# Performance work log

Measured on AMD Instinct MI355X. Metric: run time of the kernel, lower is better.

Reference implementation:

```python
import jax, jax.numpy as jnp
import numpy as np

D_MODEL = 512
D_INNER = 1024   # expand * d_model
D_STATE = 16
D_CONV = 4
DT_RANK = 32     # ceil(d_model / 16)
N_LAYERS = 4
N_PRED_LAYERS = 2
FEAT = 128
LN_EPS = 1e-5


def _ln(x, w, b):
    m = x.mean(-1, keepdims=True)
    v = ((x - m) ** 2).mean(-1, keepdims=True)
    return (x - m) * jax.lax.rsqrt(v + LN_EPS) * w + b


def _silu(x):
    return x * jax.nn.sigmoid(x)


def _causal_conv(x, w, b):
    # depthwise causal conv1d: x (B,L,C), w (C,K), b (C,)
    K = w.shape[1]
    L = x.shape[1]
    xp = jnp.pad(x, ((0, 0), (K - 1, 0), (0, 0)))
    y = b
    for k in range(K):
        y = y + xp[:, k:k + L, :] * w[:, k]
    return y


def _mamba(x, in_w, conv_w, conv_b, xp_w, dt_w, dt_b, Alog, Dp, out_w):
    # x: (B,L,d_model)
    xz = jnp.einsum('bld,ed->ble', x, in_w)          # (B,L,2*d_inner)
    xi, z = jnp.split(xz, 2, axis=-1)
    xc = _silu(_causal_conv(xi, conv_w, conv_b))     # (B,L,d_inner)
    dbc = jnp.einsum('blc,ec->ble', xc, xp_w)        # (B,L,dt_rank+2N)
    dt = dbc[..., :DT_RANK]
    Bm = dbc[..., DT_RANK:DT_RANK + D_STATE]         # (B,L,N)
    Cm = dbc[..., DT_RANK + D_STATE:]                # (B,L,N)
    delta = jax.nn.softplus(jnp.einsum('blr,cr->blc', dt, dt_w) + dt_b)  # (B,L,d_inner)
    A = -jnp.exp(Alog)                               # (d_inner,N), negative
    dA = jnp.exp(delta[..., None] * A)               # (B,L,d_inner,N)
    dBu = delta[..., None] * Bm[:, :, None, :] * xc[..., None]

    def step(h, inp):
        dA_t, dBu_t, C_t = inp
        h = dA_t * h + dBu_t                         # (B,d_inner,N)
        y = jnp.einsum('bcn,bn->bc', h, C_t)
        return h, y

    h0 = jnp.zeros((x.shape[0], D_INNER, D_STATE), x.dtype)
    _, ys = jax.lax.scan(step, h0, (dA.transpose(1, 0, 2, 3),
                                    dBu.transpose(1, 0, 2, 3),
                                    Cm.transpose(1, 0, 2)))
    y = ys.transpose(1, 0, 2) + Dp * xc              # skip connection D*u
    y = y * _silu(z)
    return jnp.einsum('blc,dc->bld', y, out_w)


def _forward(x, inp_w, inp_b, enc_ln_w, enc_ln_b, enc_in_w, enc_conv_w, enc_conv_b,
             enc_xp_w, enc_dt_w, enc_dt_b, enc_Alog, enc_D, enc_out_w,
             fin_ln_w, fin_ln_b, prd_ln_w, prd_ln_b, prd_in_w, prd_conv_w, prd_conv_b,
             prd_xp_w, prd_dt_w, prd_dt_b, prd_Alog, prd_D, prd_out_w,
             prd_nrm_w, prd_nrm_b, prd_proj_w, prd_proj_b):
    # MambaEncoder: input_proj + n_layers pre-norm residual Mamba blocks + final LN
    h = jnp.einsum('blf,df->bld', x, inp_w) + inp_b
    for i in range(N_LAYERS):
        h = h + _mamba(_ln(h, enc_ln_w[i], enc_ln_b[i]),
                       enc_in_w[i], enc_conv_w[i], enc_conv_b[i], enc_xp_w[i],
                       enc_dt_w[i], enc_dt_b[i], enc_Alog[i], enc_D[i], enc_out_w[i])
    ctx = _ln(h, fin_ln_w, fin_ln_b)
    # MambaPredictor: small causal mamba stack + norm + proj
    p = ctx
    for i in range(N_PRED_LAYERS):
        p = p + _mamba(_ln(p, prd_ln_w[i], prd_ln_b[i]),
                       prd_in_w[i], prd_conv_w[i], prd_conv_b[i], prd_xp_w[i],
                       prd_dt_w[i], prd_dt_b[i], prd_Alog[i], prd_D[i], prd_out_w[i])
    p = _ln(p, prd_nrm_w, prd_nrm_b)
    preds = jnp.einsum('bld,ed->ble', p, prd_proj_w) + prd_proj_b
    return preds


def _mamba_params(key, n, scale=0.02):
    ks = jax.random.split(key, 6)
    arange_A = jnp.tile(jnp.log(jnp.arange(1, D_STATE + 1, dtype=jnp.float32)), (n, D_INNER, 1))
    return dict(
        in_w=jax.random.normal(ks[0], (n, 2 * D_INNER, D_MODEL)) * scale,
        conv_w=jax.random.normal(ks[1], (n, D_INNER, D_CONV)) * scale,
        conv_b=jnp.zeros((n, D_INNER)),
        xp_w=jax.random.normal(ks[2], (n, DT_RANK + 2 * D_STATE, D_INNER)) * scale,
        dt_w=jax.random.normal(ks[3], (n, D_INNER, DT_RANK)) * scale,
        dt_b=jnp.full((n, D_INNER), jnp.log(jnp.expm1(0.01))),  # inv-softplus(0.01)
        Alog=arange_A,
        D=jnp.ones((n, D_INNER)),
        out_w=jax.random.normal(ks[4], (n, D_MODEL, D_INNER)) * scale,
    )


def setup_inputs() -> dict:
    key = jax.random.key(0)
    ks = jax.random.split(key, 8)
    enc = _mamba_params(ks[0], N_LAYERS)
    prd = _mamba_params(ks[1], N_PRED_LAYERS)
    return {
        'x': jax.random.normal(ks[2], (2, 1024, FEAT), dtype=jnp.float32),
        'inp_w': jax.random.normal(ks[3], (D_MODEL, FEAT)) * 0.02,
        'inp_b': jnp.zeros((D_MODEL,)),
        'enc_ln_w': jnp.ones((N_LAYERS, D_MODEL)), 'enc_ln_b': jnp.zeros((N_LAYERS, D_MODEL)),
        'enc_in_w': enc['in_w'], 'enc_conv_w': enc['conv_w'], 'enc_conv_b': enc['conv_b'],
        'enc_xp_w': enc['xp_w'], 'enc_dt_w': enc['dt_w'], 'enc_dt_b': enc['dt_b'],
        'enc_Alog': enc['Alog'], 'enc_D': enc['D'], 'enc_out_w': enc['out_w'],
        'fin_ln_w': jnp.ones((D_MODEL,)), 'fin_ln_b': jnp.zeros((D_MODEL,)),
        'prd_ln_w': jnp.ones((N_PRED_LAYERS, D_MODEL)), 'prd_ln_b': jnp.zeros((N_PRED_LAYERS, D_MODEL)),
        'prd_in_w': prd['in_w'], 'prd_conv_w': prd['conv_w'], 'prd_conv_b': prd['conv_b'],
        'prd_xp_w': prd['xp_w'], 'prd_dt_w': prd['dt_w'], 'prd_dt_b': prd['dt_b'],
        'prd_Alog': prd['Alog'], 'prd_D': prd['D'], 'prd_out_w': prd['out_w'],
        'prd_nrm_w': jnp.ones((D_MODEL,)), 'prd_nrm_b': jnp.zeros((D_MODEL,)),
        'prd_proj_w': jax.random.normal(ks[4], (D_MODEL, D_MODEL)) * 0.02,
        'prd_proj_b': jnp.zeros((D_MODEL,)),
    }


def reference(x, inp_w, inp_b, enc_ln_w, enc_ln_b, enc_in_w, enc_conv_w, enc_conv_b,
              enc_xp_w, enc_dt_w, enc_dt_b, enc_Alog, enc_D, enc_out_w,
              fin_ln_w, fin_ln_b, prd_ln_w, prd_ln_b, prd_in_w, prd_conv_w, prd_conv_b,
              prd_xp_w, prd_dt_w, prd_dt_b, prd_Alog, prd_D, prd_out_w,
              prd_nrm_w, prd_nrm_b, prd_proj_w, prd_proj_b):
    return _forward(x, inp_w, inp_b, enc_ln_w, enc_ln_b, enc_in_w, enc_conv_w, enc_conv_b,
                    enc_xp_w, enc_dt_w, enc_dt_b, enc_Alog, enc_D, enc_out_w,
                    fin_ln_w, fin_ln_b, prd_ln_w, prd_ln_b, prd_in_w, prd_conv_w, prd_conv_b,
                    prd_xp_w, prd_dt_w, prd_dt_b, prd_Alog, prd_D, prd_out_w,
                    prd_nrm_w, prd_nrm_b, prd_proj_w, prd_proj_b)
```

## Files before the change

### kernel.cpp

```cpp
#include <hip/hip_runtime.h>
#include <hip/hip_bf16.h>

using bf16 = __hip_bfloat16;
typedef __attribute__((ext_vector_type(8))) short short8;
typedef __attribute__((ext_vector_type(4))) float f32x4;

static constexpr int LB = 2;
static constexpr int LL = 1024;
static constexpr int DM = 512;
static constexpr int DI = 1024;
static constexpr int DSN = 16;
static constexpr int RK = 32;
static constexpr int MR_ROWS = LB * LL;

static constexpr int NCHUNK = 64;
static constexpr int CH = LL / NCHUNK;

__device__ __forceinline__ void gload16(const void* g, void* l) {
    __builtin_amdgcn_global_load_lds(
        (__attribute__((address_space(1))) void*)(g),
        (__attribute__((address_space(3))) void*)(l), 16, 0, 0);
}

struct ConvArgs {
    const float* src[9];
    bf16*        dst[9];
    int          n4[9];
};

__global__ __launch_bounds__(256) void convert_bf16_multi(ConvArgs a) {
    const int s = blockIdx.y;
    const float4* __restrict__ src = (const float4*)a.src[s];
    bf16* __restrict__ dst = a.dst[s];
    const int n4 = a.n4[s];
    for (int i = blockIdx.x * 256 + threadIdx.x; i < n4; i += gridDim.x * 256) {
        float4 v = src[i];
        bf16 t[4] = {__float2bfloat16(v.x), __float2bfloat16(v.y),
                     __float2bfloat16(v.z), __float2bfloat16(v.w)};
        *(uint2*)(dst + (size_t)i * 4) = *(uint2*)t;
    }
}

__global__ __launch_bounds__(256) void transpose_dtw(const float* __restrict__ enc_dtw,
                                                     const float* __restrict__ prd_dtw,
                                                     float* __restrict__ out) {
    const int layer = blockIdx.y;
    const float* src = (layer < 4) ? enc_dtw + (size_t)layer * DI * RK
                                   : prd_dtw + (size_t)(layer - 4) * DI * RK;
    float* dst = out + (size_t)layer * RK * DI;
    const int idx = blockIdx.x * 256 + threadIdx.x;
    const int k = idx >> 10, c = idx & (DI - 1);
    dst[idx] = src[(size_t)c * RK + k];
}

__device__ __forceinline__ void ln_store8(float* outrow, int lane,
                                          const float* v) {
    float4 a = {v[0], v[1], v[2], v[3]}, b = {v[4], v[5], v[6], v[7]};
    ((float4*)outrow)[lane] = a;
    ((float4*)outrow)[lane + 64] = b;
}
__device__ __forceinline__ void ln_store8(bf16* outrow, int lane,
                                          const float* v) {
    bf16 t0[4] = {__float2bfloat16(v[0]), __float2bfloat16(v[1]),
                  __float2bfloat16(v[2]), __float2bfloat16(v[3])};
    bf16 t1[4] = {__float2bfloat16(v[4]), __float2bfloat16(v[5]),
                  __float2bfloat16(v[6]), __float2bfloat16(v[7])};
    ((uint2*)outrow)[lane] = *(uint2*)t0;
    ((uint2*)outrow)[lane + 64] = *(uint2*)t1;
}

template <typename T>
__global__ __launch_bounds__(256) void ln_kernel(const float* __restrict__ x,
                                                 const float* __restrict__ w,
                                                 const float* __restrict__ b,
                                                 T* __restrict__ out,
                                                 float* __restrict__ dbc_zero) {
    if (dbc_zero != nullptr && blockIdx.x < 128) {
        ((float4*)dbc_zero)[blockIdx.x * 256 + threadIdx.x] =
            make_float4(0.f, 0.f, 0.f, 0.f);
    }
    const int wid = threadIdx.x >> 6, lane = threadIdx.x & 63;
    const int row = blockIdx.x * 4 + wid;
    const float4* xr = (const float4*)(x + (size_t)row * DM);
    const float4 v0 = xr[lane], v1 = xr[lane + 64];

    float s = (v0.x + v0.y + v0.z + v0.w) + (v1.x + v1.y + v1.z + v1.w);
#pragma unroll
    for (int m = 1; m < 64; m <<= 1) s += __shfl_xor(s, m);
    const float mean = s * (1.f / DM);

    float d[8] = {v0.x - mean, v0.y - mean, v0.z - mean, v0.w - mean,
                  v1.x - mean, v1.y - mean, v1.z - mean, v1.w - mean};
    float s2 = 0.f;
#pragma unroll
    for (int q = 0; q < 8; ++q) s2 += d[q] * d[q];
#pragma unroll
    for (int m = 1; m < 64; m <<= 1) s2 += __shfl_xor(s2, m);
    const float rs = rsqrtf(s2 * (1.f / DM) + 1e-5f);

    const float4 w0 = ((const float4*)w)[lane], w1 = ((const float4*)w)[lane + 64];
    const float4 b0 = ((const float4*)b)[lane], b1 = ((const float4*)b)[lane + 64];
    float o[8] = {d[0] * rs * w0.x + b0.x, d[1] * rs * w0.y + b0.y,
                  d[2] * rs * w0.z + b0.z, d[3] * rs * w0.w + b0.w,
                  d[4] * rs * w1.x + b1.x, d[5] * rs * w1.y + b1.y,
                  d[6] * rs * w1.z + b1.z, d[7] * rs * w1.w + b1.w};
    ln_store8(out + (size_t)row * DM, lane, o);
}

template <int BM, int BN, int BK, int EPI>
__global__ __launch_bounds__(256) void gemm_bt(const bf16* __restrict__ A, int lda,
                                               const bf16* __restrict__ B, int ldb,
                                               float* __restrict__ C, int ldc,
                                               int K, const float* __restrict__ bias) {
    static_assert(BK == 64, "layout assumes 128B LDS row");
    static_assert(BM % 32 == 0 && BN % 32 == 0, "wave staging granularity");
    constexpr int MR = (BM / 2) / 16;
    constexpr int NR = (BN / 2) / 16;
    __shared__ __align__(16) char sA[BM * 128];
    __shared__ __align__(16) char sB[BN * 128];

    const int tid = threadIdx.x;
    const int lane = tid & 63, wid = tid >> 6;
    const int wr = wid >> 1, wc = wid & 1;
    const int m0 = blockIdx.y * BM, n0 = blockIdx.x * BN;
    const int kbase = (EPI == 2) ? blockIdx.z * K : 0;

    f32x4 acc[MR][NR] = {};

    const int lrow = lane >> 3;
    const int lcol = (lane & 7) ^ lrow;
    const size_t lda2 = (size_t)lda * 2, ldb2 = (size_t)ldb * 2;
    const char* Ab = (const char*)A + (size_t)(m0 + wid * (BM / 4) + lrow) * lda2
                     + lcol * 16 + (size_t)kbase * 2;
    const char* Bb = (const char*)B + (size_t)(n0 + wid * (BN / 4) + lrow) * ldb2
                     + lcol * 16 + (size_t)kbase * 2;
    char* sAw = sA + wid * (BM / 4) * 128;
    char* sBw = sB + wid * (BN / 4) * 128;

    for (int k0 = 0; k0 < K; k0 += BK) {
#pragma unroll
        for (int i = 0; i < BM / 32; ++i)
            gload16(Ab + (size_t)i * 8 * lda2 + (size_t)k0 * 2, sAw + i * 1024);
#pragma unroll
        for (int i = 0; i < BN / 32; ++i)
            gload16(Bb + (size_t)i * 8 * ldb2 + (size_t)k0 * 2, sBw + i * 1024);
        __syncthreads();
#pragma unroll
        for (int kk = 0; kk < BK; kk += 32) {
            const int kb2 = (kk + (lane >> 4) * 8) * 2;
            short8 af[MR], bfr[NR];
#pragma unroll
            for (int m = 0; m < MR; ++m) {
                const int r = wr * (BM / 2) + m * 16 + (lane & 15);
                af[m] = *(const short8*)(sA + r * 128 + (kb2 ^ ((r & 7) << 4)));
            }
#pragma unroll
            for (int n = 0; n < NR; ++n) {
                const int r = wc * (BN / 2) + n * 16 + (lane & 15);
                bfr[n] = *(const short8*)(sB + r * 128 + (kb2 ^ ((r & 7) << 4)));
            }
#pragma unroll
            for (int m = 0; m < MR; ++m) {
#pragma unroll
                for (int n = 0; n < NR; ++n) {
                    acc[m][n] = __builtin_amdgcn_mfma_f32_16x16x32_bf16(af[m], bfr[n], acc[m][n], 0, 0, 0);
                }
            }
        }
        __syncthreads();
    }

#pragma unroll
    for (int m = 0; m < MR; ++m) {
#pragma unroll
        for (int n = 0; n < NR; ++n) {
            const int col = n0 + wc * (BN / 2) + n * 16 + (lane & 15);
            const float bv = (EPI == 1) ? bias[col] : 0.f;
#pragma unroll
            for (int j = 0; j < 4; ++j) {
                const int row = m0 + wr * (BM / 2) + m * 16 + (lane >> 4) * 4 + j;
                float v = acc[m][n][j] + bv;
                if (EPI == 4) {
                    ((bf16*)C)[(size_t)row * ldc + col] = __float2bfloat16(v);
                } else {
                    float* p = C + (size_t)row * ldc + col;
                    if (EPI == 2) {
                        atomicAdd(p, v);
                    } else {
                        if (EPI == 3) v += *p;
                        *p = v;
                    }
                }
            }
        }
    }
}

__global__ __launch_bounds__(256) void conv_silu_b(const bf16* __restrict__ xzb,
                                                   const float* __restrict__ cw,
                                                   const float* __restrict__ cb,
                                                   bf16* __restrict__ xc_bf) {
    const int idx = blockIdx.x * 256 + threadIdx.x;
    const int c = idx & (DI - 1);
    const int r = idx >> 10;
    const int l = r & (LL - 1);
    const bf16* xi = xzb + (size_t)r * (2 * DI) + c;
    const float4 w = *(const float4*)(cw + (size_t)c * 4);
    float acc = cb[c] + w.w * __bfloat162float(xi[0]);
    if (l >= 1) acc += w.z * __bfloat162float(xi[-(2 * DI)]);
    if (l >= 2) acc += w.y * __bfloat162float(xi[-(4 * DI)]);
    if (l >= 3) acc += w.x * __bfloat162float(xi[-(6 * DI)]);
    const float s = acc / (1.f + expf(-acc));
    xc_bf[idx] = __float2bfloat16(s);
}

__global__ __launch_bounds__(256) void scan_part1(const bf16* __restrict__ xcb,
                                                  const float* __restrict__ dbc,
                                                  const float* __restrict__ Alog,
                                                  const float* __restrict__ dtw_t,
                                                  const float* __restrict__ dtb,
                                                  float* __restrict__ psum,
                                                  float* __restrict__ ssum) {
    const int lane = threadIdx.x & 63;
    const int wsub = threadIdx.x >> 6;
    const int c = blockIdx.x * 64 + lane;
    const int chunk = blockIdx.y * 4 + wsub;
    const int b = blockIdx.z;
    const int r0 = b * LL + chunk * CH;

    float wv[RK];
#pragma unroll
    for (int k = 0; k < RK; ++k) wv[k] = dtw_t[(size_t)k * DI + c];
    const float bdt = dtb[c];

    float a2[DSN];
#pragma unroll
    for (int q = 0; q < 4; ++q) {
        const float4 al = *(const float4*)(Alog + (size_t)c * DSN + q * 4);
        a2[q * 4 + 0] = -expf(al.x) * 1.44269504f;
        a2[q * 4 + 1] = -expf(al.y) * 1.44269504f;
        a2[q * 4 + 2] = -expf(al.z) * 1.44269504f;
        a2[q * 4 + 3] = -expf(al.w) * 1.44269504f;
    }

    float h[DSN], P[DSN];
#pragma unroll
    for (int n = 0; n < DSN; ++n) { h[n] = 0.f; P[n] = 1.f; }

    for (int t = 0; t < CH; ++t) {
        const size_t r = r0 + t;
        float acc = bdt;
#pragma unroll
        for (int q = 0; q < RK / 4; ++q) {
            const float4 d4 = *(const float4*)(dbc + r * 64 + q * 4);
            acc = fmaf(d4.x, wv[q * 4 + 0], acc);
            acc = fmaf(d4.y, wv[q * 4 + 1], acc);
            acc = fmaf(d4.z, wv[q * 4 + 2], acc);
            acc = fmaf(d4.w, wv[q * 4 + 3], acc);
        }
        const float d = (acc > 20.f) ? acc : log1pf(expf(acc));

        const float xv = __bfloat162float(xcb[r * DI + c]);
        const float dxv = d * xv;
        float Bv[DSN];
#pragma unroll
        for (int q = 0; q < 4; ++q)
            *(float4*)&Bv[q * 4] = *(const float4*)(dbc + r * 64 + 32 + q * 4);
#pragma unroll
        for (int n = 0; n < DSN; ++n) {
            const float dA = exp2f(d * a2[n]);
            h[n] = fmaf(dA, h[n], dxv * Bv[n]);
            P[n] *= dA;
        }
    }

    const size_t obase = ((size_t)(b * NCHUNK + chunk) * DSN) * DI + c;
#pragma unroll
    for (int n = 0; n < DSN; ++n) {
        psum[obase + (size_t)n * DI] = P[n];
        ssum[obase + (size_t)n * DI] = h[n];
    }
}

__global__ __launch_bounds__(256) void scan_combine(float* __restrict__ psum,
                                                    const float* __restrict__ ssum) {
    const int lane = threadIdx.x & 63;
    const int idx = blockIdx.y * 4 + (threadIdx.x >> 6);
    const int b = idx >> 4, n = idx & 15;
    const int c = blockIdx.x * 64 + lane;
    const size_t base = ((size_t)(b * NCHUNK) * DSN + n) * DI + c;
    const size_t stride = (size_t)DSN * DI;

    float h = 0.f;
    for (int j0 = 0; j0 < NCHUNK; j0 += 8) {
        float Pv[8], Sv[8];
#pragma unroll
        for (int u = 0; u < 8; ++u) {
            Pv[u] = psum[base + (j0 + u) * stride];
            Sv[u] = ssum[base + (j0 + u) * stride];
        }
#pragma unroll
        for (int u = 0; u < 8; ++u) {
            psum[base + (j0 + u) * stride] = h;
            h = fmaf(Pv[u], h, Sv[u]);
        }
    }
}

__global__ __launch_bounds__(256) void scan_part3(const bf16* __restrict__ xcb,
                                                  const bf16* __restrict__ xzb,
                                                  const float* __restrict__ dbc,
                                                  const float* __restrict__ Alog,
                                                  const float* __restrict__ dtw_t,
                                                  const float* __restrict__ dtb,
                                                  const float* __restrict__ Dp,
                                                  const float* __restrict__ hin,
                                                  bf16* __restrict__ yg) {
    const int lane = threadIdx.x & 63;
    const int wsub = threadIdx.x >> 6;
    const int c = blockIdx.x * 64 + lane;
    const int chunk = blockIdx.y * 4 + wsub;
    const int b = blockIdx.z;
    const int r0 = b * LL + chunk * CH;

    float wv[RK];
#pragma unroll
    for (int k = 0; k < RK; ++k) wv[k] = dtw_t[(size_t)k * DI + c];
    const float bdt = dtb[c];

    float a2[DSN];
#pragma unroll
    for (int q = 0; q < 4; ++q) {
        const float4 al = *(const float4*)(Alog + (size_t)c * DSN + q * 4);
        a2[q * 4 + 0] = -expf(al.x) * 1.44269504f;
        a2[q * 4 + 1] = -expf(al.y) * 1.44269504f;
        a2[q * 4 + 2] = -expf(al.z) * 1.44269504f;
        a2[q * 4 + 3] = -expf(al.w) * 1.44269504f;
    }
    const float dp = Dp[c];

    float h[DSN];
    const size_t hbase = ((size_t)(b * NCHUNK + chunk) * DSN) * DI + c;
#pragma unroll
    for (int n = 0; n < DSN; ++n) h[n] = hin[hbase + (size_t)n * DI];

    for (int t = 0; t < CH; ++t) {
        const size_t r = r0 + t;
        float acc = bdt;
#pragma unroll
        for (int q = 0; q < RK / 4; ++q) {
            const float4 d4 = *(const float4*)(dbc + r * 64 + q * 4);
            acc = fmaf(d4.x, wv[q * 4 + 0], acc);
            acc = fmaf(d4.y, wv[q * 4 + 1], acc);
            acc = fmaf(d4.z, wv[q * 4 + 2], acc);
            acc = fmaf(d4.w, wv[q * 4 + 3], acc);
        }
        const float d = (acc > 20.f) ? acc : log1pf(expf(acc));

        const float xv = __bfloat162float(xcb[r * DI + c]);
        const float zv = __bfloat162float(xzb[r * (2 * DI) + DI + c]);
        const float dxv = d * xv;
        float Bv[DSN], Cv[DSN];
#pragma unroll
        for (int q = 0; q < 4; ++q) {
            *(float4*)&Bv[q * 4] = *(const float4*)(dbc + r * 64 + 32 + q * 4);
            *(float4*)&Cv[q * 4] = *(const float4*)(dbc + r * 64 + 48 + q * 4);
        }
        float y0 = 0.f, y1 = 0.f, y2 = 0.f, y3 = 0.f;
#pragma unroll
        for (int q = 0; q < 4; ++q) {
            {
                const float dA = exp2f(d * a2[q * 4 + 0]);
                h[q * 4 + 0] = fmaf(dA, h[q * 4 + 0], dxv * Bv[q * 4 + 0]);
                y0 = fmaf(h[q * 4 + 0], Cv[q * 4 + 0], y0);
            }
            {
                const float dA = exp2f(d * a2[q * 4 + 1]);
                h[q * 4 + 1] = fmaf(dA, h[q * 4 + 1], dxv * Bv[q * 4 + 1]);
                y1 = fmaf(h[q * 4 + 1], Cv[q * 4 + 1], y1);
            }
            {
                const float dA = exp2f(d * a2[q * 4 + 2]);
                h[q * 4 + 2] = fmaf(dA, h[q * 4 + 2], dxv * Bv[q * 4 + 2]);
                y2 = fmaf(h[q * 4 + 2], Cv[q * 4 + 2], y2);
            }
            {
                const float dA = exp2f(d * a2[q * 4 + 3]);
                h[q * 4 + 3] = fmaf(dA, h[q * 4 + 3], dxv * Bv[q * 4 + 3]);
                y3 = fmaf(h[q * 4 + 3], Cv[q * 4 + 3], y3);
            }
        }
        const float y = (y0 + y1) + (y2 + y3);
        const float zs = zv / (1.f + expf(-zv));
        yg[r * DI + c] = __float2bfloat16((y + dp * xv) * zs);
    }
}

static void run_mamba_layer(hipStream_t stream, float* resid,
                            const float* ln_w, const float* ln_b,
                            const bf16* inw_bf,
                            const float* conv_w, const float* conv_b,
                            const bf16* xpw_bf,
                            const float* dtw_t, const float* dt_b,
                            const float* Alog, const float* Dp,
                            const bf16* outw_bf,
                            bf16* ln_bf, bf16* xzb, bf16* xc_bf, float* dbc,
                            float* psum, float* ssum, bf16* yg_bf) {
    ln_kernel<bf16><<<MR_ROWS / 4, 256, 0, stream>>>(resid, ln_w, ln_b, ln_bf, dbc);
    gemm_bt<64, 64, 64, 4><<<dim3(2 * DI / 64, MR_ROWS / 64), 256, 0, stream>>>(
        ln_bf, DM, inw_bf, DM, (float*)xzb, 2 * DI, DM, nullptr);
    conv_silu_b<<<MR_ROWS * DI / 256, 256, 0, stream>>>(xzb, conv_w, conv_b, xc_bf);
    gemm_bt<32, 64, 64, 2><<<dim3(1, MR_ROWS / 32, 4), 256, 0, stream>>>(
        xc_bf, DI, xpw_bf, DI, dbc, 64, DI / 4, nullptr);
    scan_part1<<<dim3(DI / 64, NCHUNK / 4, LB), 256, 0, stream>>>(
        xc_bf, dbc, Alog, dtw_t, dt_b, psum, ssum);
    scan_combine<<<dim3(DI / 64, (LB * DSN) / 4), 256, 0, stream>>>(psum, ssum);
    scan_part3<<<dim3(DI / 64, NCHUNK / 4, LB), 256, 0, stream>>>(
        xc_bf, xzb, dbc, Alog, dtw_t, dt_b, Dp, psum, yg_bf);
    gemm_bt<32, 64, 64, 3><<<dim3(DM / 64, MR_ROWS / 32), 256, 0, stream>>>(
        yg_bf, DI, outw_bf, DI, resid, DM, DI, nullptr);
}

extern "C" void kernel_launch(void* const* d_in, const int* in_sizes, int n_in,
                              void* d_out, int out_size, void* d_ws, size_t ws_size,
                              hipStream_t stream) {
    const float* x         = (const float*)d_in[0];
    const float* inp_w     = (const float*)d_in[1];
    const float* inp_b     = (const float*)d_in[2];
    const float* enc_ln_w  = (const float*)d_in[3];
    const float* enc_ln_b  = (const float*)d_in[4];
    const float* enc_in_w  = (const float*)d_in[5];
    const float* enc_conv_w= (const float*)d_in[6];
    const float* enc_conv_b= (const float*)d_in[7];
    const float* enc_xp_w  = (const float*)d_in[8];
    const float* enc_dt_w  = (const float*)d_in[9];
    const float* enc_dt_b  = (const float*)d_in[10];
    const float* enc_Alog  = (const float*)d_in[11];
    const float* enc_D     = (const float*)d_in[12];
    const float* enc_out_w = (const float*)d_in[13];
    const float* fin_ln_w  = (const float*)d_in[14];
    const float* fin_ln_b  = (const float*)d_in[15];
    const float* prd_ln_w  = (const float*)d_in[16];
    const float* prd_ln_b  = (const float*)d_in[17];
    const float* prd_in_w  = (const float*)d_in[18];
    const float* prd_conv_w= (const float*)d_in[19];
    const float* prd_conv_b= (const float*)d_in[20];
    const float* prd_xp_w  = (const float*)d_in[21];
    const float* prd_dt_w  = (const float*)d_in[22];
    const float* prd_dt_b  = (const float*)d_in[23];
    const float* prd_Alog  = (const float*)d_in[24];
    const float* prd_D     = (const float*)d_in[25];
    const float* prd_out_w = (const float*)d_in[26];
    const float* prd_nrm_w = (const float*)d_in[27];
    const float* prd_nrm_b = (const float*)d_in[28];
    const float* prd_proj_w= (const float*)d_in[29];
    const float* prd_proj_b= (const float*)d_in[30];

    char* wp = (char*)d_ws;
    auto carve = [&](size_t elems, size_t esz) {
        void* p = (void*)wp;
        wp += (elems * esz + 255) & ~(size_t)255;
        return p;
    };
    bf16* x_bf     = (bf16*)carve((size_t)MR_ROWS * 128, 2);
    bf16* inpw_bf  = (bf16*)carve((size_t)DM * 128, 2);
    bf16* einw_bf  = (bf16*)carve(4ull * 2 * DI * DM, 2);
    bf16* expw_bf  = (bf16*)carve(4ull * 64 * DI, 2);
    bf16* eoutw_bf = (bf16*)carve(4ull * DM * DI, 2);
    bf16* pinw_bf  = (bf16*)carve(2ull * 2 * DI * DM, 2);
    bf16* pxpw_bf  = (bf16*)carve(2ull * 64 * DI, 2);
    bf16* poutw_bf = (bf16*)carve(2ull * DM * DI, 2);
    bf16* projw_bf = (bf16*)carve((size_t)DM * DM, 2);
    float* dtwt    = (float*)carve(6ull * RK * DI, 4);
    float* hbuf    = (float*)carve((size_t)MR_ROWS * DM, 4);
    float* pbuf    = (float*)carve((size_t)MR_ROWS * DM, 4);
    bf16* ln_bf    = (bf16*)carve((size_t)MR_ROWS * DM, 2);
    bf16* xzb      = (bf16*)carve((size_t)MR_ROWS * 2 * DI, 2);
    bf16* xc_bf    = (bf16*)carve((size_t)MR_ROWS * DI, 2);
    float* dbc     = (float*)carve((size_t)MR_ROWS * 64, 4);
    float* psum    = (float*)carve((size_t)LB * NCHUNK * DSN * DI, 4);
    float* ssum    = (float*)carve((size_t)LB * NCHUNK * DSN * DI, 4);
    bf16* yg_bf    = (bf16*)carve((size_t)MR_ROWS * DI, 2);

    ConvArgs ca;
    const float* csrc[9] = {x, inp_w, enc_in_w, enc_xp_w, enc_out_w,
                            prd_in_w, prd_xp_w, prd_out_w, prd_proj_w};
    bf16* cdst[9] = {x_bf, inpw_bf, einw_bf, expw_bf, eoutw_bf,
                     pinw_bf, pxpw_bf, poutw_bf, projw_bf};
    const int cn[9] = {MR_ROWS * 128, DM * 128, 4 * 2 * DI * DM, 4 * 64 * DI, 4 * DM * DI,
                       2 * 2 * DI * DM, 2 * 64 * DI, 2 * DM * DI, DM * DM};
    for (int i = 0; i < 9; ++i) { ca.src[i] = csrc[i]; ca.dst[i] = cdst[i]; ca.n4[i] = cn[i] / 4; }
    convert_bf16_multi<<<dim3(128, 9), 256, 0, stream>>>(ca);
    transpose_dtw<<<dim3(RK * DI / 256, 6), 256, 0, stream>>>(enc_dt_w, prd_dt_w, dtwt);

    gemm_bt<32, 64, 64, 1><<<dim3(DM / 64, MR_ROWS / 32), 256, 0, stream>>>(
        x_bf, 128, inpw_bf, 128, hbuf, DM, 128, inp_b);

    for (int i = 0; i < 4; ++i) {
        run_mamba_layer(stream, hbuf,
                        enc_ln_w + (size_t)i * DM, enc_ln_b + (size_t)i * DM,
                        einw_bf + (size_t)i * 2 * DI * DM,
                        enc_conv_w + (size_t)i * DI * 4, enc_conv_b + (size_t)i * DI,
                        expw_bf + (size_t)i * 64 * DI,
                        dtwt + (size_t)i * RK * DI, enc_dt_b + (size_t)i * DI,
                        enc_Alog + (size_t)i * DI * DSN, enc_D + (size_t)i * DI,
                        eoutw_bf + (size_t)i * DM * DI,
                        ln_bf, xzb, xc_bf, dbc, psum, ssum, yg_bf);
    }

    ln_kernel<float><<<MR_ROWS / 4, 256, 0, stream>>>(hbuf, fin_ln_w, fin_ln_b, pbuf, nullptr);

    for (int i = 0; i < 2; ++i) {
        run_mamba_layer(stream, pbuf,
                        prd_ln_w + (size_t)i * DM, prd_ln_b + (size_t)i * DM,
                        pinw_bf + (size_t)i * 2 * DI * DM,
                        prd_conv_w + (size_t)i * DI * 4, prd_conv_b + (size_t)i * DI,
                        pxpw_bf + (size_t)i * 64 * DI,
                        dtwt + (size_t)(4 + i) * RK * DI, prd_dt_b + (size_t)i * DI,
                        prd_Alog + (size_t)i * DI * DSN, prd_D + (size_t)i * DI,
                        poutw_bf + (size_t)i * DM * DI,
                        ln_bf, xzb, xc_bf, dbc, psum, ssum, yg_bf);
    }

    ln_kernel<bf16><<<MR_ROWS / 4, 256, 0, stream>>>(pbuf, prd_nrm_w, prd_nrm_b, ln_bf, nullptr);
    gemm_bt<32, 64, 64, 1><<<dim3(DM / 64, MR_ROWS / 32), 256, 0, stream>>>(
        ln_bf, DM, projw_bf, DM, (float*)d_out, DM, DM, prd_proj_b);

    (void)in_sizes; (void)n_in; (void)out_size; (void)ws_size;
}
```

Before: 660.6 us.

## Fuse conv, x_proj GEMM and chunked scan into one cooperative persistent kernel

Replaces five launches per layer (conv+silu, split-K x_proj GEMM, scan part1, combine, part3) with a single cooperative kernel of 512 blocks that runs each stage in turn, with grid.sync between stages. The dbc zeroing moves from the layernorm kernel into the fused kernel. The aim is to remove launch overhead and inter-kernel gaps across six layers. In exchange, grid-wide barriers add cost, the x_proj stage now uses small 16-row tiles with one loading wave, and the grid is fixed at 512 blocks, so it must stay co-resident (launch bounds set to two blocks per CU).

```diff
diff --git a/kernel.cpp b/kernel.cpp
--- a/kernel.cpp
+++ b/kernel.cpp
@@ -1,5 +1,8 @@
 #include <hip/hip_runtime.h>
 #include <hip/hip_bf16.h>
+#include <hip/hip_cooperative_groups.h>
+
+namespace cg = cooperative_groups;
 
 using bf16 = __hip_bfloat16;
 typedef __attribute__((ext_vector_type(8))) short short8;
@@ -73,12 +76,7 @@
 __global__ __launch_bounds__(256) void ln_kernel(const float* __restrict__ x,
                                                  const float* __restrict__ w,
                                                  const float* __restrict__ b,
-                                                 T* __restrict__ out,
-                                                 float* __restrict__ dbc_zero) {
-    if (dbc_zero != nullptr && blockIdx.x < 128) {
-        ((float4*)dbc_zero)[blockIdx.x * 256 + threadIdx.x] =
-            make_float4(0.f, 0.f, 0.f, 0.f);
-    }
+                                                 T* __restrict__ out) {
     const int wid = threadIdx.x >> 6, lane = threadIdx.x & 63;
     const int row = blockIdx.x * 4 + wid;
     const float4* xr = (const float4*)(x + (size_t)row * DM);
@@ -123,7 +121,6 @@
     const int lane = tid & 63, wid = tid >> 6;
     const int wr = wid >> 1, wc = wid & 1;
     const int m0 = blockIdx.y * BM, n0 = blockIdx.x * BN;
-    const int kbase = (EPI == 2) ? blockIdx.z * K : 0;
 
     f32x4 acc[MR][NR] = {};
 
@@ -131,9 +128,9 @@
     const int lcol = (lane & 7) ^ lrow;
     const size_t lda2 = (size_t)lda * 2, ldb2 = (size_t)ldb * 2;
     const char* Ab = (const char*)A + (size_t)(m0 + wid * (BM / 4) + lrow) * lda2
-                     + lcol * 16 + (size_t)kbase * 2;
+                     + lcol * 16;
     const char* Bb = (const char*)B + (size_t)(n0 + wid * (BN / 4) + lrow) * ldb2
-                     + lcol * 16 + (size_t)kbase * 2;
+                     + lcol * 16;
     char* sAw = sA + wid * (BM / 4) * 128;
     char* sBw = sB + wid * (BN / 4) * 128;
 
@@ -184,215 +181,261 @@
                     ((bf16*)C)[(size_t)row * ldc + col] = __float2bfloat16(v);
                 } else {
                     float* p = C + (size_t)row * ldc + col;
-                    if (EPI == 2) {
-                        atomicAdd(p, v);
-                    } else {
-                        if (EPI == 3) v += *p;
-                        *p = v;
-                    }
-                }
-            }
-        }
-    }
-}
-
-__global__ __launch_bounds__(256) void conv_silu_b(const bf16* __restrict__ xzb,
-                                                   const float* __restrict__ cw,
-                                                   const float* __restrict__ cb,
-                                                   bf16* __restrict__ xc_bf) {
-    const int idx = blockIdx.x * 256 + threadIdx.x;
-    const int c = idx & (DI - 1);
-    const int r = idx >> 10;
-    const int l = r & (LL - 1);
-    const bf16* xi = xzb + (size_t)r * (2 * DI) + c;
-    const float4 w = *(const float4*)(cw + (size_t)c * 4);
-    float acc = cb[c] + w.w * __bfloat162float(xi[0]);
-    if (l >= 1) acc += w.z * __bfloat162float(xi[-(2 * DI)]);
-    if (l >= 2) acc += w.y * __bfloat162float(xi[-(4 * DI)]);
-    if (l >= 3) acc += w.x * __bfloat162float(xi[-(6 * DI)]);
-    const float s = acc / (1.f + expf(-acc));
-    xc_bf[idx] = __float2bfloat16(s);
-}
-
-__global__ __launch_bounds__(256) void scan_part1(const bf16* __restrict__ xcb,
-                                                  const float* __restrict__ dbc,
-                                                  const float* __restrict__ Alog,
-                                                  const float* __restrict__ dtw_t,
-                                                  const float* __restrict__ dtb,
-                                                  float* __restrict__ psum,
-                                                  float* __restrict__ ssum) {
-    const int lane = threadIdx.x & 63;
-    const int wsub = threadIdx.x >> 6;
-    const int c = blockIdx.x * 64 + lane;
-    const int chunk = blockIdx.y * 4 + wsub;
-    const int b = blockIdx.z;
-    const int r0 = b * LL + chunk * CH;
-
-    float wv[RK];
-#pragma unroll
-    for (int k = 0; k < RK; ++k) wv[k] = dtw_t[(size_t)k * DI + c];
-    const float bdt = dtb[c];
-
-    float a2[DSN];
-#pragma unroll
-    for (int q = 0; q < 4; ++q) {
-        const float4 al = *(const float4*)(Alog + (size_t)c * DSN + q * 4);
-        a2[q * 4 + 0] = -expf(al.x) * 1.44269504f;
-        a2[q * 4 + 1] = -expf(al.y) * 1.44269504f;
-        a2[q * 4 + 2] = -expf(al.z) * 1.44269504f;
-        a2[q * 4 + 3] = -expf(al.w) * 1.44269504f;
-    }
-
-    float h[DSN], P[DSN];
-#pragma unroll
-    for (int n = 0; n < DSN; ++n) { h[n] = 0.f; P[n] = 1.f; }
-
-    for (int t = 0; t < CH; ++t) {
-        const size_t r = r0 + t;
-        float acc = bdt;
-#pragma unroll
-        for (int q = 0; q < RK / 4; ++q) {
-            const float4 d4 = *(const float4*)(dbc + r * 64 + q * 4);
-            acc = fmaf(d4.x, wv[q * 4 + 0], acc);
-            acc = fmaf(d4.y, wv[q * 4 + 1], acc);
-            acc = fmaf(d4.z, wv[q * 4 + 2], acc);
-            acc = fmaf(d4.w, wv[q * 4 + 3], acc);
-        }
-        const float d = (acc > 20.f) ? acc : log1pf(expf(acc));
-
-        const float xv = __bfloat162float(xcb[r * DI + c]);
-        const float dxv = d * xv;
-        float Bv[DSN];
-#pragma unroll
-        for (int q = 0; q < 4; ++q)
-            *(float4*)&Bv[q * 4] = *(const float4*)(dbc + r * 64 + 32 + q * 4);
+                    if (EPI == 3) v += *p;
+                    *p = v;
+                }
+            }
+        }
+    }
+}
+
+__global__ __launch_bounds__(256, 2) void mamba_inner(
+    const bf16* __restrict__ xzb, const float* __restrict__ cw,
+    const float* __restrict__ cb, const bf16* __restrict__ xpw,
+    bf16* __restrict__ xc_bf, float* __restrict__ dbc,
+    const float* __restrict__ Alog, const float* __restrict__ dtw_t,
+    const float* __restrict__ dtb, const float* __restrict__ Dp,
+    float* __restrict__ psum, float* __restrict__ ssum,
+    bf16* __restrict__ yg) {
+    cg::grid_group grid = cg::this_grid();
+    const int bid = blockIdx.x;
+    const int tid = threadIdx.x;
+    const int lane = tid & 63, wid = tid >> 6;
+
+    __shared__ __align__(16) char sA[16 * 128];
+    __shared__ __align__(16) char sB[64 * 128];
+
+    {
+        if (bid < 128) {
+            ((float4*)dbc)[bid * 256 + tid] = make_float4(0.f, 0.f, 0.f, 0.f);
+        }
+        const int base = bid * 256 + tid;
+        const int c = base & (DI - 1);
+        const int r00 = base >> 10;
+        const float4 w = *(const float4*)(cw + (size_t)c * 4);
+        const float cbv = cb[c];
+#pragma unroll
+        for (int i = 0; i < 16; ++i) {
+            const int r = r00 + i * 128;
+            const int l = r & (LL - 1);
+            const bf16* xi = xzb + (size_t)r * (2 * DI) + c;
+            float acc = cbv + w.w * __bfloat162float(xi[0]);
+            if (l >= 1) acc += w.z * __bfloat162float(xi[-(2 * DI)]);
+            if (l >= 2) acc += w.y * __bfloat162float(xi[-(4 * DI)]);
+            if (l >= 3) acc += w.x * __bfloat162float(xi[-(6 * DI)]);
+            const float s = acc / (1.f + expf(-acc));
+            xc_bf[(size_t)r * DI + c] = __float2bfloat16(s);
+        }
+    }
+    grid.sync();
+
+    {
+        const int mt = bid & 127, kc = bid >> 7;
+        const int m0 = mt * 16;
+        const int kbase = kc * 256;
+        const int lrow = lane >> 3, lcol8 = lane & 7;
+        f32x4 acc = {};
+        for (int k0 = kbase; k0 < kbase + 256; k0 += 64) {
+            if (wid == 0) {
+#pragma unroll
+                for (int i = 0; i < 2; ++i) {
+                    const int ri = i * 8 + lrow;
+                    const int ci = lcol8 ^ lrow;
+                    gload16((const char*)xc_bf + (size_t)(m0 + ri) * (DI * 2)
+                                + (size_t)k0 * 2 + ci * 16,
+                            sA + i * 1024);
+                }
+            }
+#pragma unroll
+            for (int i = 0; i < 2; ++i) {
+                const int ri = wid * 16 + i * 8 + lrow;
+                const int ci = lcol8 ^ lrow;
+                gload16((const char*)xpw + (size_t)ri * (DI * 2)
+                            + (size_t)k0 * 2 + ci * 16,
+                        sB + (wid * 16 + i * 8) * 128);
+            }
+            __syncthreads();
+#pragma unroll
+            for (int kk = 0; kk < 64; kk += 32) {
+                const int kb2 = (kk + (lane >> 4) * 8) * 2;
+                const int ra = lane & 15;
+                const short8 af = *(const short8*)(sA + ra * 128 + (kb2 ^ ((ra & 7) << 4)));
+                const int rb = wid * 16 + (lane & 15);
+                const short8 bfr = *(const short8*)(sB + rb * 128 + (kb2 ^ ((rb & 7) << 4)));
+                acc = __builtin_amdgcn_mfma_f32_16x16x32_bf16(af, bfr, acc, 0, 0, 0);
+            }
+            __syncthreads();
+        }
+        const int col = wid * 16 + (lane & 15);
+#pragma unroll
+        for (int j = 0; j < 4; ++j) {
+            const int row = m0 + (lane >> 4) * 4 + j;
+            atomicAdd(&dbc[(size_t)row * 64 + col], acc[j]);
+        }
+    }
+    grid.sync();
+
+    {
+        const int cb_ = bid & 15, cg_ = (bid >> 4) & 15, b = bid >> 8;
+        const int c = cb_ * 64 + lane;
+        const int chunk = cg_ * 4 + wid;
+        const int r0 = b * LL + chunk * CH;
+
+        float wv[RK];
+#pragma unroll
+        for (int k = 0; k < RK; ++k) wv[k] = dtw_t[(size_t)k * DI + c];
+        const float bdt = dtb[c];
+
+        float a2[DSN];
+#pragma unroll
+        for (int q = 0; q < 4; ++q) {
+            const float4 al = *(const float4*)(Alog + (size_t)c * DSN + q * 4);
+            a2[q * 4 + 0] = -expf(al.x) * 1.44269504f;
+            a2[q * 4 + 1] = -expf(al.y) * 1.44269504f;
+            a2[q * 4 + 2] = -expf(al.z) * 1.44269504f;
+            a2[q * 4 + 3] = -expf(al.w) * 1.44269504f;
+        }
+
+        float h[DSN], P[DSN];
+#pragma unroll
+        for (int n = 0; n < DSN; ++n) { h[n] = 0.f; P[n] = 1.f; }
+
+        for (int t = 0; t < CH; ++t) {
+            const size_t r = r0 + t;
+            float acc = bdt;
+#pragma unroll
+            for (int q = 0; q < RK / 4; ++q) {
+                const float4 d4 = *(const float4*)(dbc + r * 64 + q * 4);
+                acc = fmaf(d4.x, wv[q * 4 + 0], acc);
+                acc = fmaf(d4.y, wv[q * 4 + 1], acc);
+                acc = fmaf(d4.z, wv[q * 4 + 2], acc);
+                acc = fmaf(d4.w, wv[q * 4 + 3], acc);
+            }
+            const float d = (acc > 20.f) ? acc : log1pf(expf(acc));
+            const float xv = __bfloat162float(xc_bf[r * DI + c]);
+            const float dxv = d * xv;
+            float Bv[DSN];
+#pragma unroll
+            for (int q = 0; q < 4; ++q)
+                *(float4*)&Bv[q * 4] = *(const float4*)(dbc + r * 64 + 32 + q * 4);
+#pragma unroll
+            for (int n = 0; n < DSN; ++n) {
+                const float dA = exp2f(d * a2[n]);
+                h[n] = fmaf(dA, h[n], dxv * Bv[n]);
+                P[n] *= dA;
+            }
+        }
+
+        const size_t obase = ((size_t)(b * NCHUNK + chunk) * DSN) * DI + c;
 #pragma unroll
         for (int n = 0; n < DSN; ++n) {
-            const float dA = exp2f(d * a2[n]);
-            h[n] = fmaf(dA, h[n], dxv * Bv[n]);
-            P[n] *= dA;
-        }
-    }
-
-    const size_t obase = ((size_t)(b * NCHUNK + chunk) * DSN) * DI + c;
-#pragma unroll
-    for (int n = 0; n < DSN; ++n) {
-        psum[obase + (size_t)n * DI] = P[n];
-        ssum[obase + (size_t)n * DI] = h[n];
-    }
-}
-
-__global__ __launch_bounds__(256) void scan_combine(float* __restrict__ psum,
-                                                    const float* __restrict__ ssum) {
-    const int lane = threadIdx.x & 63;
-    const int idx = blockIdx.y * 4 + (threadIdx.x >> 6);
-    const int b = idx >> 4, n = idx & 15;
-    const int c = blockIdx.x * 64 + lane;
-    const size_t base = ((size_t)(b * NCHUNK) * DSN + n) * DI + c;
-    const size_t stride = (size_t)DSN * DI;
-
-    float h = 0.f;
-    for (int j0 = 0; j0 < NCHUNK; j0 += 8) {
-        float Pv[8], Sv[8];
-#pragma unroll
-        for (int u = 0; u < 8; ++u) {
-            Pv[u] = psum[base + (j0 + u) * stride];
-            Sv[u] = ssum[base + (j0 + u) * stride];
-        }
-#pragma unroll
-        for (int u = 0; u < 8; ++u) {
-            psum[base + (j0 + u) * stride] = h;
-            h = fmaf(Pv[u], h, Sv[u]);
-        }
-    }
-}
-
-__global__ __launch_bounds__(256) void scan_part3(const bf16* __restrict__ xcb,
-                                                  const bf16* __restrict__ xzb,
-                                                  const float* __restrict__ dbc,
-                                                  const float* __restrict__ Alog,
-                                                  const float* __restrict__ dtw_t,
-                                                  const float* __restrict__ dtb,
-                                                  const float* __restrict__ Dp,
-                                                  const float* __restrict__ hin,
-                                                  bf16* __restrict__ yg) {
-    const int lane = threadIdx.x & 63;
-    const int wsub = threadIdx.x >> 6;
-    const int c = blockIdx.x * 64 + lane;
-    const int chunk = blockIdx.y * 4 + wsub;
-    const int b = blockIdx.z;
-    const int r0 = b * LL + chunk * CH;
-
-    float wv[RK];
-#pragma unroll
-    for (int k = 0; k < RK; ++k) wv[k] = dtw_t[(size_t)k * DI + c];
-    const float bdt = dtb[c];
-
-    float a2[DSN];
-#pragma unroll
-    for (int q = 0; q < 4; ++q) {
-        const float4 al = *(const float4*)(Alog + (size_t)c * DSN + q * 4);
-        a2[q * 4 + 0] = -expf(al.x) * 1.44269504f;
-        a2[q * 4 + 1] = -expf(al.y) * 1.44269504f;
-        a2[q * 4 + 2] = -expf(al.z) * 1.44269504f;
-        a2[q * 4 + 3] = -expf(al.w) * 1.44269504f;
-    }
-    const float dp = Dp[c];
-
-    float h[DSN];
-    const size_t hbase = ((size_t)(b * NCHUNK + chunk) * DSN) * DI + c;
-#pragma unroll
-    for (int n = 0; n < DSN; ++n) h[n] = hin[hbase + (size_t)n * DI];
-
-    for (int t = 0; t < CH; ++t) {
-        const size_t r = r0 + t;
-        float acc = bdt;
-#pragma unroll
-        for (int q = 0; q < RK / 4; ++q) {
-            const float4 d4 = *(const float4*)(dbc + r * 64 + q * 4);
-            acc = fmaf(d4.x, wv[q * 4 + 0], acc);
-            acc = fmaf(d4.y, wv[q * 4 + 1], acc);
-            acc = fmaf(d4.z, wv[q * 4 + 2], acc);
-            acc = fmaf(d4.w, wv[q * 4 + 3], acc);
-        }
-        const float d = (acc > 20.f) ? acc : log1pf(expf(acc));
-
-        const float xv = __bfloat162float(xcb[r * DI + c]);
-        const float zv = __bfloat162float(xzb[r * (2 * DI) + DI + c]);
-        const float dxv = d * xv;
-        float Bv[DSN], Cv[DSN];
+            psum[obase + (size_t)n * DI] = P[n];
+            ssum[obase + (size_t)n * DI] = h[n];
+        }
+    }
+    grid.sync();
+
+    if (bid < 128) {
+        const int cb_ = bid & 15, grp = bid >> 4;
+        const int idx = grp * 4 + wid;
+        const int b = idx >> 4, n = idx & 15;
+        const int c = cb_ * 64 + lane;
+        const size_t base = ((size_t)(b * NCHUNK) * DSN + n) * DI + c;
+        const size_t stride = (size_t)DSN * DI;
+
+        float h = 0.f;
+        for (int j0 = 0; j0 < NCHUNK; j0 += 8) {
+            float Pv[8], Sv[8];
+#pragma unroll
+            for (int u = 0; u < 8; ++u) {
+                Pv[u] = psum[base + (j0 + u) * stride];
+                Sv[u] = ssum[base + (j0 + u) * stride];
+            }
+#pragma unroll
+            for (int u = 0; u < 8; ++u) {
+                psum[base + (j0 + u) * stride] = h;
+                h = fmaf(Pv[u], h, Sv[u]);
+            }
+        }
+    }
+    grid.sync();
+
+    {
+        const int cb_ = bid & 15, cg_ = (bid >> 4) & 15, b = bid >> 8;
+        const int c = cb_ * 64 + lane;
+        const int chunk = cg_ * 4 + wid;
+        const int r0 = b * LL + chunk * CH;
+
+        float wv[RK];
+#pragma unroll
+        for (int k = 0; k < RK; ++k) wv[k] = dtw_t[(size_t)k * DI + c];
+        const float bdt = dtb[c];
+
+        float a2[DSN];
 #pragma unroll
         for (int q = 0; q < 4; ++q) {
-            *(float4*)&Bv[q * 4] = *(const float4*)(dbc + r * 64 + 32 + q * 4);
-            *(float4*)&Cv[q * 4] = *(const float4*)(dbc + r * 64 + 48 + q * 4);
-        }
-        float y0 = 0.f, y1 = 0.f, y2 = 0.f, y3 = 0.f;
-#pragma unroll
-        for (int q = 0; q < 4; ++q) {
-            {
-                const float dA = exp2f(d * a2[q * 4 + 0]);
-                h[q * 4 + 0] = fmaf(dA, h[q * 4 + 0], dxv * Bv[q * 4 + 0]);
-                y0 = fmaf(h[q * 4 + 0], Cv[q * 4 + 0], y0);
-            }
-            {
-                const float dA = exp2f(d * a2[q * 4 + 1]);
-                h[q * 4 + 1] = fmaf(dA, h[q * 4 + 1], dxv * Bv[q * 4 + 1]);
-                y1 = fmaf(h[q * 4 + 1], Cv[q * 4 + 1], y1);
-            }
-            {
-                const float dA = exp2f(d * a2[q * 4 + 2]);
-                h[q * 4 + 2] = fmaf(dA, h[q * 4 + 2], dxv * Bv[q * 4 + 2]);
-                y2 = fmaf(h[q * 4 + 2], Cv[q * 4 + 2], y2);
-            }
-            {
-                const float dA = exp2f(d * a2[q * 4 + 3]);
-                h[q * 4 + 3] = fmaf(dA, h[q * 4 + 3], dxv * Bv[q * 4 + 3]);
-                y3 = fmaf(h[q * 4 + 3], Cv[q * 4 + 3], y3);
-            }
-        }
-        const float y = (y0 + y1) + (y2 + y3);
-        const float zs = zv / (1.f + expf(-zv));
-        yg[r * DI + c] = __float2bfloat16((y + dp * xv) * zs);
+            const float4 al = *(const float4*)(Alog + (size_t)c * DSN + q * 4);
+            a2[q * 4 + 0] = -expf(al.x) * 1.44269504f;
+            a2[q * 4 + 1] = -expf(al.y) * 1.44269504f;
+            a2[q * 4 + 2] = -expf(al.z) * 1.44269504f;
+            a2[q * 4 + 3] = -expf(al.w) * 1.44269504f;
+        }
+        const float dp = Dp[c];
+
+        float h[DSN];
+        const size_t hbase = ((size_t)(b * NCHUNK + chunk) * DSN) * DI + c;
+#pragma unroll
+        for (int n = 0; n < DSN; ++n) h[n] = psum[hbase + (size_t)n * DI];
+
+        for (int t = 0; t < CH; ++t) {
+            const size_t r = r0 + t;
+            float acc = bdt;
+#pragma unroll
+            for (int q = 0; q < RK / 4; ++q) {
+                const float4 d4 = *(const float4*)(dbc + r * 64 + q * 4);
+                acc = fmaf(d4.x, wv[q * 4 + 0], acc);
+                acc = fmaf(d4.y, wv[q * 4 + 1], acc);
+                acc = fmaf(d4.z, wv[q * 4 + 2], acc);
+                acc = fmaf(d4.w, wv[q * 4 + 3], acc);
+            }
+            const float d = (acc > 20.f) ? acc : log1pf(expf(acc));
+            const float xv = __bfloat162float(xc_bf[r * DI + c]);
+            const float zv = __bfloat162float(xzb[r * (2 * DI) + DI + c]);
+            const float dxv = d * xv;
+            float Bv[DSN], Cv[DSN];
+#pragma unroll
+            for (int q = 0; q < 4; ++q) {
+                *(float4*)&Bv[q * 4] = *(const float4*)(dbc + r * 64 + 32 + q * 4);
+                *(float4*)&Cv[q * 4] = *(const float4*)(dbc + r * 64 + 48 + q * 4);
+            }
+            float y0 = 0.f, y1 = 0.f, y2 = 0.f, y3 = 0.f;
+#pragma unroll
+            for (int q = 0; q < 4; ++q) {
+                {
+                    const float dA = exp2f(d * a2[q * 4 + 0]);
+                    h[q * 4 + 0] = fmaf(dA, h[q * 4 + 0], dxv * Bv[q * 4 + 0]);
+                    y0 = fmaf(h[q * 4 + 0], Cv[q * 4 + 0], y0);
+                }
+                {
+                    const float dA = exp2f(d * a2[q * 4 + 1]);
+                    h[q * 4 + 1] = fmaf(dA, h[q * 4 + 1], dxv * Bv[q * 4 + 1]);
+                    y1 = fmaf(h[q * 4 + 1], Cv[q * 4 + 1], y1);
+                }
+                {
+                    const float dA = exp2f(d * a2[q * 4 + 2]);
+                    h[q * 4 + 2] = fmaf(dA, h[q * 4 + 2], dxv * Bv[q * 4 + 2]);
+                    y2 = fmaf(h[q * 4 + 2], Cv[q * 4 + 2], y2);
+                }
+                {
+                    const float dA = exp2f(d * a2[q * 4 + 3]);
+                    h[q * 4 + 3] = fmaf(dA, h[q * 4 + 3], dxv * Bv[q * 4 + 3]);
+                    y3 = fmaf(h[q * 4 + 3], Cv[q * 4 + 3], y3);
+                }
+            }
+            const float y = (y0 + y1) + (y2 + y3);
+            const float zs = zv / (1.f + expf(-zv));
+            yg[r * DI + c] = __float2bfloat16((y + dp * xv) * zs);
+        }
     }
 }
 
@@ -406,17 +449,15 @@
                             const bf16* outw_bf,
                             bf16* ln_bf, bf16* xzb, bf16* xc_bf, float* dbc,
                             float* psum, float* ssum, bf16* yg_bf) {
-    ln_kernel<bf16><<<MR_ROWS / 4, 256, 0, stream>>>(resid, ln_w, ln_b, ln_bf, dbc);
+    ln_kernel<bf16><<<MR_ROWS / 4, 256, 0, stream>>>(resid, ln_w, ln_b, ln_bf);
     gemm_bt<64, 64, 64, 4><<<dim3(2 * DI / 64, MR_ROWS / 64), 256, 0, stream>>>(
         ln_bf, DM, inw_bf, DM, (float*)xzb, 2 * DI, DM, nullptr);
-    conv_silu_b<<<MR_ROWS * DI / 256, 256, 0, stream>>>(xzb, conv_w, conv_b, xc_bf);
-    gemm_bt<32, 64, 64, 2><<<dim3(1, MR_ROWS / 32, 4), 256, 0, stream>>>(
-        xc_bf, DI, xpw_bf, DI, dbc, 64, DI / 4, nullptr);
-    scan_part1<<<dim3(DI / 64, NCHUNK / 4, LB), 256, 0, stream>>>(
-        xc_bf, dbc, Alog, dtw_t, dt_b, psum, ssum);
-    scan_combine<<<dim3(DI / 64, (LB * DSN) / 4), 256, 0, stream>>>(psum, ssum);
-    scan_part3<<<dim3(DI / 64, NCHUNK / 4, LB), 256, 0, stream>>>(
-        xc_bf, xzb, dbc, Alog, dtw_t, dt_b, Dp, psum, yg_bf);
+    void* args[] = {(void*)&xzb, (void*)&conv_w, (void*)&conv_b, (void*)&xpw_bf,
+                    (void*)&xc_bf, (void*)&dbc, (void*)&Alog, (void*)&dtw_t,
+                    (void*)&dt_b, (void*)&Dp, (void*)&psum, (void*)&ssum,
+                    (void*)&yg_bf};
+    hipLaunchCooperativeKernel(reinterpret_cast<void*>(mamba_inner),
+                               dim3(512), dim3(256), args, 0, stream);
     gemm_bt<32, 64, 64, 3><<<dim3(DM / 64, MR_ROWS / 32), 256, 0, stream>>>(
         yg_bf, DI, outw_bf, DI, resid, DM, DI, nullptr);
 }
@@ -508,7 +549,7 @@
                         ln_bf, xzb, xc_bf, dbc, psum, ssum, yg_bf);
     }
 
-    ln_kernel<float><<<MR_ROWS / 4, 256, 0, stream>>>(hbuf, fin_ln_w, fin_ln_b, pbuf, nullptr);
+    ln_kernel<float><<<MR_ROWS / 4, 256, 0, stream>>>(hbuf, fin_ln_w, fin_ln_b, pbuf);
 
     for (int i = 0; i < 2; ++i) {
         run_mamba_layer(stream, pbuf,
@@ -522,7 +563,7 @@
                         ln_bf, xzb, xc_bf, dbc, psum, ssum, yg_bf);
     }
 
-    ln_kernel<bf16><<<MR_ROWS / 4, 256, 0, stream>>>(pbuf, prd_nrm_w, prd_nrm_b, ln_bf, nullptr);
+    ln_kernel<bf16><<<MR_ROWS / 4, 256, 0, stream>>>(pbuf, prd_nrm_w, prd_nrm_b, ln_bf);
     gemm_bt<32, 64, 64, 1><<<dim3(DM / 64, MR_ROWS / 32), 256, 0, stream>>>(
         ln_bf, DM, projw_bf, DM, (float*)d_out, DM, DM, prd_proj_b);
 
```

Result: slower. 2.046 ms (+209.8%).
